# Kernel optimization log

Measured on AMD Instinct MI355X. Metric: run time of the kernel, lower is better.

The kernel has to match this reference:

```python
import jax, jax.numpy as jnp
import numpy as np

EMBED_DIM = 1024
NUM_HEADS = 16
HEAD_DIM = EMBED_DIM // NUM_HEADS


def setup_inputs() -> dict:
    key = jax.random.key(0)
    kx, kq, kk, kv, ko = jax.random.split(key, 5)
    scale = 1.0 / np.sqrt(EMBED_DIM)
    return {
        "x": jax.random.normal(kx, (4, 2048, EMBED_DIM), dtype=jnp.float32),
        # nn.Linear weights are [out, in]; y = x @ W.T
        "w_q": jax.random.normal(kq, (EMBED_DIM, EMBED_DIM), dtype=jnp.float32) * scale,
        "w_k": jax.random.normal(kk, (EMBED_DIM, EMBED_DIM), dtype=jnp.float32) * scale,
        "w_v": jax.random.normal(kv, (EMBED_DIM, EMBED_DIM), dtype=jnp.float32) * scale,
        "w_o": jax.random.normal(ko, (EMBED_DIM, EMBED_DIM), dtype=jnp.float32) * scale,
    }


def reference(x, w_q, w_k, w_v, w_o):
    b, s, _ = x.shape
    # projections (Linear with no bias: x @ W.T)
    q = (x @ w_q.T).reshape(b, s, NUM_HEADS, HEAD_DIM).transpose(0, 2, 1, 3)
    k = (x @ w_k.T).reshape(b, s, NUM_HEADS, HEAD_DIM).transpose(0, 2, 1, 3)
    v = (x @ w_v.T).reshape(b, s, NUM_HEADS, HEAD_DIM).transpose(0, 2, 1, 3)
    # scores: [b, h, s, s]
    scores = jnp.einsum("bhqd,bhkd->bhqk", q, k) / jnp.sqrt(jnp.float32(HEAD_DIM)).astype(x.dtype)
    attn = jax.nn.softmax(scores, axis=-1)
    out = jnp.einsum("bhqk,bhkd->bhqd", attn, v)  # [b, h, s, d]
    out = out.transpose(0, 2, 1, 3).reshape(b, s, EMBED_DIM)
    return out @ w_o.T
```

## Files before the change

kernel.cpp:

```cpp
#include <hip/hip_runtime.h>
#include <math.h>

#define EMBED 1024
#define NHEAD 16
#define HDIM  64
#define BATCH 4
#define SEQ   2048
#define MROWS (BATCH * SEQ)

typedef __attribute__((ext_vector_type(4))) short short4v;
typedef __attribute__((ext_vector_type(8))) short short8;
typedef __attribute__((ext_vector_type(4))) float floatx4;
typedef __attribute__((ext_vector_type(16))) float floatx16;

#if __has_builtin(__builtin_amdgcn_exp2f)
#define EXP2(x) __builtin_amdgcn_exp2f(x)
#else
#define EXP2(x) exp2f(x)
#endif

__device__ __forceinline__ unsigned short f2bf(float f) {
  unsigned u = __float_as_uint(f);
  u += 0x7fffu + ((u >> 16) & 1u);
  return (unsigned short)(u >> 16);
}

#if __has_builtin(__builtin_amdgcn_cvt_pk_bf16_f32)
__device__ __forceinline__ unsigned pack2bf(float lo, float hi) {
  typedef __attribute__((ext_vector_type(2))) __bf16 bf2;
  union { bf2 b; unsigned u; } c;
  c.b = __builtin_amdgcn_cvt_pk_bf16_f32(lo, hi);
  return c.u;
}
#else
__device__ __forceinline__ unsigned pack2bf(float lo, float hi) {
  return ((__float_as_uint(lo) + 0x8000u) >> 16) |
         ((__float_as_uint(hi) + 0x8000u) & 0xffff0000u);
}
#endif

__device__ __forceinline__ void gl_lds16(const void* g, void* l) {
  __builtin_amdgcn_global_load_lds(
      (const __attribute__((address_space(1))) unsigned int*)g,
      (__attribute__((address_space(3))) unsigned int*)l, 16, 0, 0);
}

__global__ __launch_bounds__(256) void cast_bf16_kernel(
    const float* __restrict__ x,  const float* __restrict__ wq,
    const float* __restrict__ wk, const float* __restrict__ wv,
    const float* __restrict__ wo,
    unsigned short* __restrict__ xb, unsigned short* __restrict__ wb) {
  const size_t NX = (size_t)MROWS * EMBED;
  size_t i4 = ((size_t)blockIdx.x * 256 + threadIdx.x) * 4;
  const float* src;
  unsigned short* dst;
  size_t off;
  if (i4 < NX) {
    src = x; dst = xb; off = i4;
  } else {
    size_t j = i4 - NX;
    int r = (int)(j >> 20);
    off = j & ((1u << 20) - 1);
    src = (r == 0) ? wq : (r == 1) ? wk : (r == 2) ? wv : wo;
    dst = wb + ((size_t)r << 20);
  }
  float4 v = *(const float4*)(src + off);
  ushort4 o;
  o.x = f2bf(v.x); o.y = f2bf(v.y); o.z = f2bf(v.z); o.w = f2bf(v.w);
  *(ushort4*)(dst + off) = o;
}

__device__ __forceinline__ void gemm_core(
    const unsigned short* __restrict__ Amat,
    const unsigned short* __restrict__ Bmat,
    int mBase, int nBase,
    unsigned short* As, unsigned short* Bs,
    floatx4 acc[4][4]) {
  const int t = threadIdx.x;
  const int lane = t & 63, w = t >> 6;
  const int wr = w >> 1, wc = w & 1;
  const int quad = lane >> 4, l15 = lane & 15;

  const int f0 = (w * 2 + 0) * 64 + lane;
  const int f1 = (w * 2 + 1) * 64 + lane;
  const unsigned short* ga0 = Amat + (size_t)(mBase + (f0 >> 2)) * EMBED + (f0 & 3) * 8;
  const unsigned short* ga1 = Amat + (size_t)(mBase + (f1 >> 2)) * EMBED + (f1 & 3) * 8;
  const unsigned short* gb0 = Bmat + (size_t)(nBase + (f0 >> 2)) * EMBED + (f0 & 3) * 8;
  const unsigned short* gb1 = Bmat + (size_t)(nBase + (f1 >> 2)) * EMBED + (f1 & 3) * 8;
  unsigned short* la0 = As + (w * 2 + 0) * 512;
  unsigned short* la1 = As + (w * 2 + 1) * 512;
  unsigned short* lb0 = Bs + (w * 2 + 0) * 512;
  unsigned short* lb1 = Bs + (w * 2 + 1) * 512;

  for (int kb = 0; kb < EMBED; kb += 32) {
    __syncthreads();
    gl_lds16(ga0 + kb, la0);
    gl_lds16(ga1 + kb, la1);
    gl_lds16(gb0 + kb, lb0);
    gl_lds16(gb1 + kb, lb1);
    __syncthreads();
    short8 a[4], b[4];
#pragma unroll
    for (int mi = 0; mi < 4; ++mi)
      a[mi] = *(const short8*)&As[(wr * 64 + mi * 16 + l15) * 32 + quad * 8];
#pragma unroll
    for (int ni = 0; ni < 4; ++ni)
      b[ni] = *(const short8*)&Bs[(wc * 64 + ni * 16 + l15) * 32 + quad * 8];
#pragma unroll
    for (int mi = 0; mi < 4; ++mi)
#pragma unroll
      for (int ni = 0; ni < 4; ++ni)
        acc[mi][ni] = __builtin_amdgcn_mfma_f32_16x16x32_bf16(
            a[mi], b[ni], acc[mi][ni], 0, 0, 0);
  }
}

__global__ __launch_bounds__(256) void proj_qkv_bf16(
    const unsigned short* __restrict__ xb,
    const unsigned short* __restrict__ wb,
    unsigned short* __restrict__ qkv) {
  const int which = blockIdx.z;
  const unsigned short* W = wb + ((size_t)which << 20);
  const int nBase = blockIdx.x * 128;
  const int mBase = blockIdx.y * 128;

  __shared__ unsigned short As[128 * 32];
  __shared__ unsigned short Bs[128 * 32];

  floatx4 acc[4][4] = {};
  gemm_core(xb, W, mBase, nBase, As, Bs, acc);

  const int t = threadIdx.x;
  const int lane = t & 63, w = t >> 6;
  const int wr = w >> 1, wc = w & 1;
  const int quad = lane >> 4, l15 = lane & 15;

  unsigned short* out = qkv + (size_t)which * MROWS * EMBED;
  if (which < 2) {
    const float scale = (which == 0) ? 0.18033688f : 1.0f;
#pragma unroll
    for (int mi = 0; mi < 4; ++mi)
#pragma unroll
      for (int ni = 0; ni < 4; ++ni) {
        const int n = nBase + wc * 64 + ni * 16 + l15;
        const int h = n >> 6, d = n & 63;
#pragma unroll
        for (int r = 0; r < 4; ++r) {
          const int m = mBase + wr * 64 + mi * 16 + quad * 4 + r;
          const int b = m >> 11, s = m & (SEQ - 1);
          out[(((size_t)(b * NHEAD + h) * SEQ) + s) * HDIM + d] =
              f2bf(acc[mi][ni][r] * scale);
        }
      }
  } else {
#pragma unroll
    for (int mi = 0; mi < 4; ++mi) {
      const int m0 = mBase + wr * 64 + mi * 16 + quad * 4;
      const int b = m0 >> 11, s0 = m0 & (SEQ - 1);
#pragma unroll
      for (int ni = 0; ni < 4; ++ni) {
        const int n = nBase + wc * 64 + ni * 16 + l15;
        const int h = n >> 6, d = n & 63;
        ushort4 pk;
        pk.x = f2bf(acc[mi][ni][0]); pk.y = f2bf(acc[mi][ni][1]);
        pk.z = f2bf(acc[mi][ni][2]); pk.w = f2bf(acc[mi][ni][3]);
        *(ushort4*)&out[((size_t)(b * NHEAD + h) * HDIM + d) * SEQ + s0] = pk;
      }
    }
  }
}

__global__ __launch_bounds__(512, 2) void attn_mfma(
    const unsigned short* __restrict__ qkv,
    unsigned short* __restrict__ aout) {
  const unsigned short* Q = qkv;
  const unsigned short* K = qkv + (size_t)MROWS * EMBED;
  const unsigned short* V = qkv + 2 * (size_t)MROWS * EMBED;

  const int id = blockIdx.x;
  const int xcd = id & 7, slot = id >> 3;
  const int bh = xcd * 8 + (slot >> 2);
  const int qBase = (slot & 3) * 512;

  __shared__ unsigned short Ks[2 * 128 * 64];
  __shared__ unsigned short Vs[2 * 64 * 128];

  const int t = threadIdx.x;
  const int lane = t & 63, w = t >> 6;
  const int h2 = lane >> 5;
  const int q31 = lane & 31;

  const unsigned short* qrowA =
      Q + ((size_t)bh * SEQ + qBase + w * 64 + q31) * HDIM;
  const unsigned short* qrowB = qrowA + 32 * HDIM;
  short8 qaA[4], qaB[4];
#pragma unroll
  for (int ds = 0; ds < 4; ++ds) {
    qaA[ds] = *(const short8*)(qrowA + ds * 16 + h2 * 8);
    qaB[ds] = *(const short8*)(qrowB + ds * 16 + h2 * 8);
  }

  const unsigned short* kbase = K + (size_t)bh * SEQ * HDIM;
  const unsigned short* vbase = V + (size_t)bh * HDIM * SEQ;
  const unsigned short* gk[2];
  const unsigned short* gv[2];
  unsigned short* lk[2];
  unsigned short* lv[2];
#pragma unroll
  for (int i = 0; i < 2; ++i) {
    const int c = i * 512 + t;
    const int krow = c >> 3, kgrp = (c & 7) ^ (krow & 7);
    gk[i] = kbase + (size_t)krow * HDIM + kgrp * 8;
    const int vd = c >> 4, vj = (c & 15) ^ (vd & 15);
    gv[i] = vbase + (size_t)vd * SEQ + vj * 8;
    const int cu = i * 512 + w * 64;
    lk[i] = Ks + cu * 8;
    lv[i] = Vs + cu * 8;
  }

  floatx16 otA0 = {}, otA1 = {};
  floatx16 otB0 = {}, otB1 = {};
  float laccA = 0.0f, laccB = 0.0f;

#pragma unroll
  for (int i = 0; i < 2; ++i) {
    gl_lds16(gk[i], lk[i]);
    gl_lds16(gv[i], lv[i]);
  }

  for (int kt = 0; kt < SEQ; kt += 128) {
    const int cb = (kt >> 7) & 1;
    const int nb = cb ^ 1;
    const int nxt = (kt + 128) & (SEQ - 1);
    const int sOff = nb * 8192;
#pragma unroll
    for (int i = 0; i < 2; ++i) {
      gl_lds16(gk[i] + (size_t)nxt * HDIM, lk[i] + sOff);
      gl_lds16(gv[i] + nxt, lv[i] + sOff);
    }
    __builtin_amdgcn_sched_barrier(0);
    asm volatile("s_waitcnt vmcnt(4)" ::: "memory");
    __builtin_amdgcn_s_barrier();

    const int kOff = cb * 8192;
    const int vOff = cb * 8192;

#pragma unroll
    for (int sub = 0; sub < 2; ++sub) {
      const int koff = sub * 64;

      floatx16 stA0 = {}, stA1 = {}, stB0 = {}, stB1 = {};
      __builtin_amdgcn_s_setprio(1);
#pragma unroll
      for (int ds = 0; ds < 4; ++ds) {
        const int g = ds * 2 + h2;
        const int k0 = koff + q31;
        short8 ka0 = *(const short8*)&Ks[kOff + k0 * 64 + ((g ^ (q31 & 7)) * 8)];
        stA0 = __builtin_amdgcn_mfma_f32_32x32x16_bf16(ka0, qaA[ds], stA0, 0, 0, 0);
        stB0 = __builtin_amdgcn_mfma_f32_32x32x16_bf16(ka0, qaB[ds], stB0, 0, 0, 0);
        const int k1 = koff + 32 + q31;
        short8 ka1 = *(const short8*)&Ks[kOff + k1 * 64 + ((g ^ (q31 & 7)) * 8)];
        stA1 = __builtin_amdgcn_mfma_f32_32x32x16_bf16(ka1, qaA[ds], stA1, 0, 0, 0);
        stB1 = __builtin_amdgcn_mfma_f32_32x32x16_bf16(ka1, qaB[ds], stB1, 0, 0, 0);
      }
      __builtin_amdgcn_s_setprio(0);

      unsigned pkA0[8], pkA1[8], pkB0[8], pkB1[8];
#pragma unroll
      for (int i = 0; i < 8; ++i) {
        float a0 = EXP2(stA0[2 * i]), b0 = EXP2(stA0[2 * i + 1]);
        float a1 = EXP2(stA1[2 * i]), b1 = EXP2(stA1[2 * i + 1]);
        laccA += (a0 + b0) + (a1 + b1);
        pkA0[i] = pack2bf(a0, b0);
        pkA1[i] = pack2bf(a1, b1);
        float c0 = EXP2(stB0[2 * i]), d0 = EXP2(stB0[2 * i + 1]);
        float c1 = EXP2(stB1[2 * i]), d1 = EXP2(stB1[2 * i + 1]);
        laccB += (c0 + d0) + (c1 + d1);
        pkB0[i] = pack2bf(c0, d0);
        pkB1[i] = pack2bf(c1, d1);
      }

      __builtin_amdgcn_s_setprio(1);
#pragma unroll
      for (int s = 0; s < 8; ++s) {
        const unsigned* pkA = (s < 4) ? pkA0 : pkA1;
        const unsigned* pkB = (s < 4) ? pkB0 : pkB1;
        const int rg = s & 3;
        union { unsigned u[2]; short4v v; } pbA, pbB;
        pbA.u[0] = pkA[2 * rg + 0];
        pbA.u[1] = pkA[2 * rg + 1];
        pbB.u[0] = pkB[2 * rg + 0];
        pbB.u[1] = pkB[2 * rg + 1];

        const int g = sub * 8 + s;
        const int pos = ((g ^ (q31 & 15)) * 8) + h2 * 4;
        short4v va0 = *(const short4v*)&Vs[vOff + q31 * 128 + pos];
        otA0 = __builtin_amdgcn_mfma_f32_32x32x8bf16_1k(va0, pbA.v, otA0, 0, 0, 0);
        otB0 = __builtin_amdgcn_mfma_f32_32x32x8bf16_1k(va0, pbB.v, otB0, 0, 0, 0);
        short4v va1 = *(const short4v*)&Vs[vOff + (32 + q31) * 128 + pos];
        otA1 = __builtin_amdgcn_mfma_f32_32x32x8bf16_1k(va1, pbA.v, otA1, 0, 0, 0);
        otB1 = __builtin_amdgcn_mfma_f32_32x32x8bf16_1k(va1, pbB.v, otB1, 0, 0, 0);
      }
      __builtin_amdgcn_s_setprio(0);
    }

    __builtin_amdgcn_sched_barrier(0);
    __builtin_amdgcn_s_barrier();
  }
  asm volatile("s_waitcnt vmcnt(0)" ::: "memory");

  const float totA = laccA + __shfl_xor(laccA, 32);
  const float totB = laccB + __shfl_xor(laccB, 32);
  const float invA = 1.0f / totA;
  const float invB = 1.0f / totB;

  const int b = bh >> 4, hh = bh & 15;
  unsigned short* orowA =
      aout + ((size_t)b * SEQ + qBase + w * 64 + q31) * EMBED + hh * HDIM;
  unsigned short* orowB = orowA + (size_t)32 * EMBED;
#pragma unroll
  for (int rg = 0; rg < 4; ++rg) {
    const int d0 = rg * 8 + h2 * 4;
    ushort4 p0, p1;
    p0.x = f2bf(otA0[4 * rg + 0] * invA); p0.y = f2bf(otA0[4 * rg + 1] * invA);
    p0.z = f2bf(otA0[4 * rg + 2] * invA); p0.w = f2bf(otA0[4 * rg + 3] * invA);
    *(ushort4*)(orowA + d0) = p0;
    p1.x = f2bf(otA1[4 * rg + 0] * invA); p1.y = f2bf(otA1[4 * rg + 1] * invA);
    p1.z = f2bf(otA1[4 * rg + 2] * invA); p1.w = f2bf(otA1[4 * rg + 3] * invA);
    *(ushort4*)(orowA + 32 + d0) = p1;
    ushort4 p2, p3;
    p2.x = f2bf(otB0[4 * rg + 0] * invB); p2.y = f2bf(otB0[4 * rg + 1] * invB);
    p2.z = f2bf(otB0[4 * rg + 2] * invB); p2.w = f2bf(otB0[4 * rg + 3] * invB);
    *(ushort4*)(orowB + d0) = p2;
    p3.x = f2bf(otB1[4 * rg + 0] * invB); p3.y = f2bf(otB1[4 * rg + 1] * invB);
    p3.z = f2bf(otB1[4 * rg + 2] * invB); p3.w = f2bf(otB1[4 * rg + 3] * invB);
    *(ushort4*)(orowB + 32 + d0) = p3;
  }
}

__global__ __launch_bounds__(256) void out_proj_bf16(
    const unsigned short* __restrict__ aout,
    const unsigned short* __restrict__ wb,
    float* __restrict__ Cout) {
  const int nBase = blockIdx.x * 128;
  const int mBase = blockIdx.y * 128;

  __shared__ unsigned short As[128 * 32];
  __shared__ unsigned short Bs[128 * 32];

  floatx4 acc[4][4] = {};
  gemm_core(aout, wb + ((size_t)3 << 20), mBase, nBase, As, Bs, acc);

  const int t = threadIdx.x;
  const int lane = t & 63, w = t >> 6;
  const int wr = w >> 1, wc = w & 1;
  const int quad = lane >> 4, l15 = lane & 15;

#pragma unroll
  for (int mi = 0; mi < 4; ++mi)
#pragma unroll
    for (int ni = 0; ni < 4; ++ni) {
      const int n = nBase + wc * 64 + ni * 16 + l15;
#pragma unroll
      for (int r = 0; r < 4; ++r) {
        const int m = mBase + wr * 64 + mi * 16 + quad * 4 + r;
        Cout[(size_t)m * EMBED + n] = acc[mi][ni][r];
      }
    }
}

extern "C" void kernel_launch(void* const* d_in, const int* in_sizes, int n_in,
                              void* d_out, int out_size, void* d_ws, size_t ws_size,
                              hipStream_t stream) {
  const float* x  = (const float*)d_in[0];
  const float* wq = (const float*)d_in[1];
  const float* wk = (const float*)d_in[2];
  const float* wv = (const float*)d_in[3];
  const float* wo = (const float*)d_in[4];
  float* out = (float*)d_out;

  char* ws = (char*)d_ws;
  unsigned short* xb   = (unsigned short*)(ws);
  unsigned short* wb   = (unsigned short*)(ws + (16u << 20));
  unsigned short* qkv  = (unsigned short*)(ws + (26u << 20));
  unsigned short* aout = (unsigned short*)(ws + (76u << 20));

  cast_bf16_kernel<<<12288, 256, 0, stream>>>(x, wq, wk, wv, wo, xb, wb);
  proj_qkv_bf16<<<dim3(EMBED / 128, MROWS / 128, 3), 256, 0, stream>>>(xb, wb, qkv);
  attn_mfma<<<256, 512, 0, stream>>>(qkv, aout);
  out_proj_bf16<<<dim3(EMBED / 128, MROWS / 128), 256, 0, stream>>>(aout, wb, out);
}
```

Measured before the change: 286.4 us.

## Use 32x32x16 MFMA for PV via permlane32 swap; halve attention block size

The P·V product now uses the wider 32x32x16 bf16 MFMA instead of the older 32x32x8 variant. permlane32_swap exchanges packed probability halves between the two half-waves so the operands match the larger K layout. This halves the number of PV MFMA issues and V LDS reads per tile. Separately, the attention kernel moves from 256 blocks of 512 threads to 512 blocks of 256 threads, each covering 256 queries, with each thread issuing 4 async K/V loads per stage instead of 2. That gives more blocks for scheduling, but each block streams all K/V once, so K/V traffic doubles.

```diff
diff --git a/kernel.cpp b/kernel.cpp
--- a/kernel.cpp
+++ b/kernel.cpp
@@ -12,6 +12,7 @@
 typedef __attribute__((ext_vector_type(8))) short short8;
 typedef __attribute__((ext_vector_type(4))) float floatx4;
 typedef __attribute__((ext_vector_type(16))) float floatx16;
+typedef __attribute__((ext_vector_type(2))) unsigned uint2v;
 
 #if __has_builtin(__builtin_amdgcn_exp2f)
 #define EXP2(x) __builtin_amdgcn_exp2f(x)
@@ -38,6 +39,20 @@
          ((__float_as_uint(hi) + 0x8000u) & 0xffff0000u);
 }
 #endif
+
+__device__ __forceinline__ uint2v pl32swap(unsigned a, unsigned b) {
+#if __has_builtin(__builtin_amdgcn_permlane32_swap)
+  return __builtin_amdgcn_permlane32_swap(a, b, false, false);
+#else
+  uint2v r;
+  unsigned ax = (unsigned)__shfl_xor((int)a, 32);
+  unsigned bx = (unsigned)__shfl_xor((int)b, 32);
+  const int hi = (int)((threadIdx.x & 63) >> 5);
+  r[0] = hi ? bx : a;
+  r[1] = hi ? b : ax;
+  return r;
+#endif
+}
 
 __device__ __forceinline__ void gl_lds16(const void* g, void* l) {
   __builtin_amdgcn_global_load_lds(
@@ -170,7 +185,7 @@
   }
 }
 
-__global__ __launch_bounds__(512, 2) void attn_mfma(
+__global__ __launch_bounds__(256, 2) void attn_mfma(
     const unsigned short* __restrict__ qkv,
     unsigned short* __restrict__ aout) {
   const unsigned short* Q = qkv;
@@ -179,8 +194,8 @@
 
   const int id = blockIdx.x;
   const int xcd = id & 7, slot = id >> 3;
-  const int bh = xcd * 8 + (slot >> 2);
-  const int qBase = (slot & 3) * 512;
+  const int bh = xcd * 8 + (slot >> 3);
+  const int qBase = (slot & 7) * 256;
 
   __shared__ unsigned short Ks[2 * 128 * 64];
   __shared__ unsigned short Vs[2 * 64 * 128];
@@ -202,18 +217,18 @@
 
   const unsigned short* kbase = K + (size_t)bh * SEQ * HDIM;
   const unsigned short* vbase = V + (size_t)bh * HDIM * SEQ;
-  const unsigned short* gk[2];
-  const unsigned short* gv[2];
-  unsigned short* lk[2];
-  unsigned short* lv[2];
-#pragma unroll
-  for (int i = 0; i < 2; ++i) {
-    const int c = i * 512 + t;
+  const unsigned short* gk[4];
+  const unsigned short* gv[4];
+  unsigned short* lk[4];
+  unsigned short* lv[4];
+#pragma unroll
+  for (int i = 0; i < 4; ++i) {
+    const int c = i * 256 + t;
     const int krow = c >> 3, kgrp = (c & 7) ^ (krow & 7);
     gk[i] = kbase + (size_t)krow * HDIM + kgrp * 8;
     const int vd = c >> 4, vj = (c & 15) ^ (vd & 15);
     gv[i] = vbase + (size_t)vd * SEQ + vj * 8;
-    const int cu = i * 512 + w * 64;
+    const int cu = i * 256 + w * 64;
     lk[i] = Ks + cu * 8;
     lv[i] = Vs + cu * 8;
   }
@@ -223,7 +238,7 @@
   float laccA = 0.0f, laccB = 0.0f;
 
 #pragma unroll
-  for (int i = 0; i < 2; ++i) {
+  for (int i = 0; i < 4; ++i) {
     gl_lds16(gk[i], lk[i]);
     gl_lds16(gv[i], lv[i]);
   }
@@ -234,12 +249,12 @@
     const int nxt = (kt + 128) & (SEQ - 1);
     const int sOff = nb * 8192;
 #pragma unroll
-    for (int i = 0; i < 2; ++i) {
+    for (int i = 0; i < 4; ++i) {
       gl_lds16(gk[i] + (size_t)nxt * HDIM, lk[i] + sOff);
       gl_lds16(gv[i] + nxt, lv[i] + sOff);
     }
     __builtin_amdgcn_sched_barrier(0);
-    asm volatile("s_waitcnt vmcnt(4)" ::: "memory");
+    asm volatile("s_waitcnt vmcnt(8)" ::: "memory");
     __builtin_amdgcn_s_barrier();
 
     const int kOff = cb * 8192;
@@ -282,24 +297,26 @@
 
       __builtin_amdgcn_s_setprio(1);
 #pragma unroll
-      for (int s = 0; s < 8; ++s) {
-        const unsigned* pkA = (s < 4) ? pkA0 : pkA1;
-        const unsigned* pkB = (s < 4) ? pkB0 : pkB1;
-        const int rg = s & 3;
-        union { unsigned u[2]; short4v v; } pbA, pbB;
-        pbA.u[0] = pkA[2 * rg + 0];
-        pbA.u[1] = pkA[2 * rg + 1];
-        pbB.u[0] = pkB[2 * rg + 0];
-        pbB.u[1] = pkB[2 * rg + 1];
-
-        const int g = sub * 8 + s;
-        const int pos = ((g ^ (q31 & 15)) * 8) + h2 * 4;
-        short4v va0 = *(const short4v*)&Vs[vOff + q31 * 128 + pos];
-        otA0 = __builtin_amdgcn_mfma_f32_32x32x8bf16_1k(va0, pbA.v, otA0, 0, 0, 0);
-        otB0 = __builtin_amdgcn_mfma_f32_32x32x8bf16_1k(va0, pbB.v, otB0, 0, 0, 0);
-        short4v va1 = *(const short4v*)&Vs[vOff + (32 + q31) * 128 + pos];
-        otA1 = __builtin_amdgcn_mfma_f32_32x32x8bf16_1k(va1, pbA.v, otA1, 0, 0, 0);
-        otB1 = __builtin_amdgcn_mfma_f32_32x32x8bf16_1k(va1, pbB.v, otB1, 0, 0, 0);
+      for (int sp = 0; sp < 4; ++sp) {
+        const unsigned* pA = (sp < 2) ? pkA0 : pkA1;
+        const unsigned* pB = (sp < 2) ? pkB0 : pkB1;
+        const int off = (sp & 1) * 4;
+        uint2v ra0 = pl32swap(pA[off + 0], pA[off + 2]);
+        uint2v ra1 = pl32swap(pA[off + 1], pA[off + 3]);
+        uint2v rb0 = pl32swap(pB[off + 0], pB[off + 2]);
+        uint2v rb1 = pl32swap(pB[off + 1], pB[off + 3]);
+        union { unsigned u[4]; short8 v; } pbA, pbB;
+        pbA.u[0] = ra0[0]; pbA.u[1] = ra1[0]; pbA.u[2] = ra0[1]; pbA.u[3] = ra1[1];
+        pbB.u[0] = rb0[0]; pbB.u[1] = rb1[0]; pbB.u[2] = rb0[1]; pbB.u[3] = rb1[1];
+
+        const int g8 = sub * 8 + sp * 2 + h2;
+        const int pos = (g8 ^ (q31 & 15)) * 8;
+        short8 va0 = *(const short8*)&Vs[vOff + q31 * 128 + pos];
+        otA0 = __builtin_amdgcn_mfma_f32_32x32x16_bf16(va0, pbA.v, otA0, 0, 0, 0);
+        otB0 = __builtin_amdgcn_mfma_f32_32x32x16_bf16(va0, pbB.v, otB0, 0, 0, 0);
+        short8 va1 = *(const short8*)&Vs[vOff + (32 + q31) * 128 + pos];
+        otA1 = __builtin_amdgcn_mfma_f32_32x32x16_bf16(va1, pbA.v, otA1, 0, 0, 0);
+        otB1 = __builtin_amdgcn_mfma_f32_32x32x16_bf16(va1, pbB.v, otB1, 0, 0, 0);
       }
       __builtin_amdgcn_s_setprio(0);
     }
@@ -387,6 +404,6 @@
 
   cast_bf16_kernel<<<12288, 256, 0, stream>>>(x, wq, wk, wv, wo, xb, wb);
   proj_qkv_bf16<<<dim3(EMBED / 128, MROWS / 128, 3), 256, 0, stream>>>(xb, wb, qkv);
-  attn_mfma<<<256, 512, 0, stream>>>(qkv, aout);
+  attn_mfma<<<512, 256, 0, stream>>>(qkv, aout);
   out_proj_bf16<<<dim3(EMBED / 128, MROWS / 128), 256, 0, stream>>>(aout, wb, out);
 }
```

Result: faster. 279.1 us (-2.6%).
